# Kernel optimization log

Hardware: AMD Instinct MI355X
Metric: run time of the kernel (lower is better)

The kernel has to match this reference:

```python
import jax, jax.numpy as jnp
import numpy as np

NUM_SITES = 64
BOND_DIM = 64
PHYS_DIM = 2
BATCH = 8192
INIT_STD = 0.125  # 1/sqrt(bond_dim)
EPS_AMP = 1e-12
EPS_LOG = 1e-30


def setup_inputs() -> dict:
    key = jax.random.key(0)
    k_cfg, k_l, k_b, k_r = jax.random.split(key, 4)
    configurations = jax.random.randint(k_cfg, (BATCH, NUM_SITES), 0, PHYS_DIM, dtype=jnp.int32)
    left = jax.random.normal(k_l, (PHYS_DIM, BOND_DIM), dtype=jnp.float32) * INIT_STD
    bulk = jax.random.normal(k_b, (NUM_SITES - 2, BOND_DIM, PHYS_DIM, BOND_DIM), dtype=jnp.float32) * INIT_STD
    right = jax.random.normal(k_r, (BOND_DIM, PHYS_DIM), dtype=jnp.float32) * INIT_STD
    return {"configurations": configurations, "left": left, "bulk": bulk, "right": right}


def _psi(configurations, left, bulk, right):
    # configurations: [B, S] int; left: [d, D]; bulk: [S-2, D, d, D]; right: [D, d]
    B = configurations.shape[0]
    env0 = left[configurations[:, 0]]  # [B, D]
    cfg_mid = configurations[:, 1:-1].T  # [S-2, B]

    def step(env, xs):
        site_t, idx = xs  # site_t: [D, d, D], idx: [B]
        D = site_t.shape[0]
        # env @ site (contract left bond), then gather the per-sample physical slice
        tmp = (env @ site_t.reshape(D, -1)).reshape(B, PHYS_DIM, D)  # [B, d, D]
        env = jnp.take_along_axis(tmp, idx[:, None, None], axis=1)[:, 0, :]  # [B, D]
        return env, None

    env, _ = jax.lax.scan(step, env0, (bulk, cfg_mid))
    cols = jnp.take(right, configurations[:, -1], axis=1).T  # [B, D]
    return jnp.sum(env * cols, axis=1)  # [B]


def _log_norm(left, bulk, right):
    env0 = left.T @ left  # [D, D]  (real dtype -> conj trivial)

    def step(carry, site_t):
        env, log_scale = carry
        sm = jnp.transpose(site_t, (1, 0, 2))  # [d, D, D]
        env = jnp.einsum('pdi,de,pej->ij', sm, env, sm)  # sum_p A_p^H env A_p
        scale = jnp.maximum(jnp.max(jnp.abs(env)), EPS_LOG)
        return (env / scale, log_scale + jnp.log(scale)), None

    (env, log_scale), _ = jax.lax.scan(step, (env0, jnp.zeros((), left.dtype)), bulk)
    z = jnp.sum(right * (env @ right))
    return jnp.log(jnp.maximum(z, EPS_LOG)) + log_scale


def reference(configurations, left, bulk, right):
    psi = _psi(configurations, left, bulk, right)
    abs_sq = jnp.maximum(psi * psi, EPS_AMP)
    log_z = _log_norm(left, bulk, right)
    nll = -(jnp.log(abs_sq) - log_z)
    return jnp.mean(nll)
```

## Files before the change

kernel.cpp:

```cpp
#include <hip/hip_runtime.h>
#include <math.h>

#define NBULK 62
#define NBLK  130

typedef __attribute__((ext_vector_type(8))) short bf8_t;
typedef __attribute__((ext_vector_type(4))) float f4_t;

#define MFMA(a, b, c) __builtin_amdgcn_mfma_f32_16x16x32_bf16((a), (b), (c), 0, 0, 0)
#define LGKM_BARRIER() asm volatile("s_waitcnt lgkmcnt(0)\n\ts_barrier" ::: "memory")

__device__ __forceinline__ unsigned short f2bf(float f) {
    unsigned int u = __float_as_uint(f);
    return (unsigned short)((u + 0x7FFFu + ((u >> 16) & 1u)) >> 16);
}
__device__ __forceinline__ float bf2f(unsigned short h) {
    return __uint_as_float(((unsigned int)h) << 16);
}
__device__ __forceinline__ void gload16(const void* g, void* l) {
    __builtin_amdgcn_global_load_lds(
        (const __attribute__((address_space(1))) unsigned int*)g,
        (__attribute__((address_space(3))) unsigned int*)l, 16, 0, 0);
}

#define WS_E_OFF   1024
#define WS_B_OFF   6144
#define WS_BT_OFF  45056
#define WS_MR_OFF  1060864

extern "C" __global__ __launch_bounds__(256)
void mps_precompute(const float* __restrict__ bulkG,
                    unsigned short* __restrict__ BTg,
                    unsigned short* __restrict__ MRg,
                    float* __restrict__ wsF)
{
    __shared__ unsigned short BTl[8192];
    __shared__ unsigned short MRl[8192];
    const int s = blockIdx.x, tid = threadIdx.x;
    if (s == 0 && tid == 0) {
        wsF[0] = 0.f; wsF[1] = 0.f; wsF[2] = 0.f;
        ((int*)wsF)[3] = 0;
    }
    const float4* src = (const float4*)(bulkG + (size_t)s * 8192);
    for (int c = 0; c < 8; ++c) {
        int idx = tid + c * 256;
        float4 v = src[idx];
        int f  = idx * 4;
        int kk = f >> 7;
        int p  = (f >> 6) & 1;
        int j  = f & 63;
        unsigned short b0 = f2bf(v.x), b1 = f2bf(v.y), b2 = f2bf(v.z), b3 = f2bf(v.w);
        int n = p * 64 + kk;
        int off = n * 64 + (((j >> 3) ^ (n & 7)) << 3) + (j & 7);
        MRl[off + 0] = b0; MRl[off + 1] = b1; MRl[off + 2] = b2; MRl[off + 3] = b3;
        unsigned short bb[4] = {b0, b1, b2, b3};
        #pragma unroll
        for (int t2 = 0; t2 < 4; ++t2) {
            int n2 = p * 64 + j + t2;
            BTl[n2 * 64 + (((kk >> 3) ^ (n2 & 7)) << 3) + (kk & 7)] = bb[t2];
        }
    }
    __syncthreads();
    const uint4* bt4 = (const uint4*)BTl;
    const uint4* mr4 = (const uint4*)MRl;
    uint4* btg = (uint4*)(BTg + (size_t)s * 8192);
    uint4* mrg = (uint4*)(MRg + (size_t)s * 8192);
    for (int c = 0; c < 4; ++c) {
        int idx = tid + c * 256;
        btg[idx] = bt4[idx];
        mrg[idx] = mr4[idx];
    }
}

extern "C" __global__ __launch_bounds__(256, 1)
void mps_main(const int* __restrict__ cfgG, const float* __restrict__ leftG,
              const float* __restrict__ rightG, float* __restrict__ wsF,
              const unsigned short* __restrict__ BTg,
              const unsigned short* __restrict__ MRg,
              float* __restrict__ outG)
{
    extern __shared__ char smem[];
    unsigned short* smem16 = (unsigned short*)smem;
    const int tid  = threadIdx.x;
    const int bid  = blockIdx.x;
    const int wv   = tid >> 6;
    const int lane = tid & 63;
    const int quad = lane >> 4;
    const int ln   = lane & 15;
    const int swz  = ln & 7;

    if (bid >= 2) {
        unsigned short* Tb0 = smem16;
        unsigned short* Tb1 = Tb0 + 8192;
        unsigned short* env = Tb1 + 8192;

        const int s0  = (bid - 2) * 64;
        const int sMy = wv * 16 + ln;
        const int esw = (sMy & 7) << 3;
        unsigned short* eb = env + sMy * 64;

        unsigned long long SEL = 0ull;
        {
            const int* row = cfgG + (size_t)(s0 + sMy) * 64;
            #pragma unroll
            for (int q = 0; q < 16; ++q) {
                int4 v = *(const int4*)(row + q * 4);
                SEL |= ((unsigned long long)(v.x & 1)) << (q * 4);
                SEL |= ((unsigned long long)(v.y & 1)) << (q * 4 + 1);
                SEL |= ((unsigned long long)(v.z & 1)) << (q * 4 + 2);
                SEL |= ((unsigned long long)(v.w & 1)) << (q * 4 + 3);
            }
        }
        {
            const char* g0 = (const char*)BTg;
            for (int c = 0; c < 4; ++c) {
                int chunk = wv * 4 + c;
                gload16(g0 + chunk * 1024 + (size_t)lane * 16, (char*)Tb0 + chunk * 1024);
            }
        }
        bf8_t Ef0, Ef1;
        {
            int sel0 = (int)(SEL & 1ull);
            const float* lp = leftG + sel0 * 64;
            bf8_t t0, t1;
            #pragma unroll
            for (int j = 0; j < 8; ++j) {
                t0[j] = (short)f2bf(lp[quad * 8 + j]);
                t1[j] = (short)f2bf(lp[32 + quad * 8 + j]);
            }
            Ef0 = t0; Ef1 = t1;
        }

        for (int t = 0; t < NBULK; ++t) {
            __syncthreads();
            unsigned short* Tl = (t & 1) ? Tb1 : Tb0;
            if (t + 1 < NBULK) {
                const char* gn = (const char*)(BTg + (size_t)(t + 1) * 8192);
                char* l = (char*)((t & 1) ? Tb0 : Tb1);
                for (int c = 0; c < 4; ++c) {
                    int chunk = wv * 4 + c;
                    gload16(gn + chunk * 1024 + (size_t)lane * 16, l + chunk * 1024);
                }
            }
            f4_t a0[4], a1[4];
            #pragma unroll
            for (int mt = 0; mt < 4; ++mt) {
                const unsigned short* r0 = Tl + (mt * 16 + ln) * 64;
                const unsigned short* r1 = Tl + (64 + mt * 16 + ln) * 64;
                bf8_t A00 = *(const bf8_t*)(r0 + ((quad       ^ swz) << 3));
                bf8_t A01 = *(const bf8_t*)(r0 + (((4 + quad) ^ swz) << 3));
                bf8_t A10 = *(const bf8_t*)(r1 + ((quad       ^ swz) << 3));
                bf8_t A11 = *(const bf8_t*)(r1 + (((4 + quad) ^ swz) << 3));
                f4_t x = {0.f, 0.f, 0.f, 0.f};
                x = MFMA(A00, Ef0, x);
                x = MFMA(A01, Ef1, x);
                a0[mt] = x;
                f4_t y = {0.f, 0.f, 0.f, 0.f};
                y = MFMA(A10, Ef0, y);
                y = MFMA(A11, Ef1, y);
                a1[mt] = y;
            }
            const bool bs = ((SEL >> (t + 1)) & 1ull) != 0ull;
            #pragma unroll
            for (int mt = 0; mt < 4; ++mt) {
                ushort4 pk;
                pk.x = f2bf(bs ? a1[mt][0] : a0[mt][0]);
                pk.y = f2bf(bs ? a1[mt][1] : a0[mt][1]);
                pk.z = f2bf(bs ? a1[mt][2] : a0[mt][2]);
                pk.w = f2bf(bs ? a1[mt][3] : a0[mt][3]);
                *(ushort4*)(eb + ((mt * 16 + quad * 4) ^ esw)) = pk;
            }
            Ef0 = *(const bf8_t*)(eb + ((quad * 8)      ^ esw));
            Ef1 = *(const bf8_t*)(eb + ((quad * 8 + 32) ^ esw));
        }
        {
            const int selL = (int)((SEL >> 63) & 1ull);
            float p = 0.f;
            #pragma unroll
            for (int g2 = 0; g2 < 2; ++g2) {
                int g = quad * 2 + g2;
                bf8_t e = *(const bf8_t*)(eb + ((g * 8) ^ esw));
                #pragma unroll
                for (int j = 0; j < 8; ++j)
                    p = fmaf(bf2f((unsigned short)e[j]), rightG[(g * 8 + j) * 2 + selL], p);
            }
            p += __shfl_xor(p, 16);
            p += __shfl_xor(p, 32);
            float lp = logf(fmaxf(p * p, 1e-12f));
            lp += __shfl_xor(lp, 1); lp += __shfl_xor(lp, 2);
            lp += __shfl_xor(lp, 4); lp += __shfl_xor(lp, 8);
            if (lane == 0) atomicAdd(&wsF[0], lp);
        }
    } else {
        unsigned short* Tb0 = smem16;
        unsigned short* Tb1 = Tb0 + 8192;
        unsigned short* E   = Tb1 + 8192;
        unsigned short* St  = E + 4096;
        float* wred = (float*)(St + 8192);

        const bool fwd = (bid == 0);
        const unsigned short* srcbase = fwd ? BTg : MRg;
        {
            int i = tid >> 2, jq = tid & 3;
            for (int jj = 0; jj < 16; ++jj) {
                int j = jq * 16 + jj;
                float v;
                if (fwd) v = leftG[i] * leftG[j] + leftG[64 + i] * leftG[64 + j];
                else     v = rightG[i * 2] * rightG[j * 2] + rightG[i * 2 + 1] * rightG[j * 2 + 1];
                E[i * 64 + (j ^ ((i & 7) << 3))] = f2bf(v);
            }
        }
        {
            int st = fwd ? 0 : 61;
            const char* g = (const char*)(srcbase + (size_t)st * 8192);
            for (int c = 0; c < 4; ++c) {
                int chunk = wv * 4 + c;
                gload16(g + chunk * 1024 + (size_t)lane * 16, (char*)Tb0 + chunk * 1024);
            }
        }
        float lsum = 0.f;
        const int p   = wv >> 1;
        const int ntb = (wv & 1) * 2;
        const int mta = (wv >> 1) * 2;
        const int nta = (wv & 1) * 2;

        for (int k = 0; k < 31; ++k) {
            __syncthreads();
            unsigned short* Tl = (k & 1) ? Tb1 : Tb0;
            if (k + 1 < 31) {
                int sn = fwd ? (k + 1) : (61 - (k + 1));
                const char* g = (const char*)(srcbase + (size_t)sn * 8192);
                char* l = (char*)((k & 1) ? Tb0 : Tb1);
                for (int c = 0; c < 4; ++c) {
                    int chunk = wv * 4 + c;
                    gload16(g + chunk * 1024 + (size_t)lane * 16, l + chunk * 1024);
                }
            }
            float inv = 1.f;
            if (k > 0) {
                const float* wp = wred + ((k - 1) & 1) * 4;
                float mm = fmaxf(fmaxf(wp[0], wp[1]), fmaxf(wp[2], wp[3]));
                float sc = fmaxf(mm, 1e-30f);
                inv = 1.f / sc;
                if (tid == 0) lsum += logf(sc);
            }
            {
                bf8_t Bf[2][2];
                #pragma unroll
                for (int c = 0; c < 2; ++c) {
                    const unsigned short* rb = Tl + (p * 64 + (ntb + c) * 16 + ln) * 64;
                    Bf[c][0] = *(const bf8_t*)(rb + ((quad       ^ swz) << 3));
                    Bf[c][1] = *(const bf8_t*)(rb + (((4 + quad) ^ swz) << 3));
                }
                #pragma unroll
                for (int it = 0; it < 4; ++it) {
                    const unsigned short* er = E + (it * 16 + ln) * 64;
                    bf8_t A0 = *(const bf8_t*)(er + ((quad * 8)      ^ (swz << 3)));
                    bf8_t A1 = *(const bf8_t*)(er + ((quad * 8 + 32) ^ (swz << 3)));
                    #pragma unroll
                    for (int c = 0; c < 2; ++c) {
                        f4_t x = {0.f, 0.f, 0.f, 0.f};
                        x = MFMA(A0, Bf[c][0], x);
                        x = MFMA(A1, Bf[c][1], x);
                        int n = (ntb + c) * 16 + ln;
                        ushort4 pk;
                        pk.x = f2bf(x[0]); pk.y = f2bf(x[1]); pk.z = f2bf(x[2]); pk.w = f2bf(x[3]);
                        *(ushort4*)(St + p * 4096 + n * 64 + ((it * 16 + quad * 4) ^ ((n & 7) << 3))) = pk;
                    }
                }
            }
            LGKM_BARRIER();
            {
                f4_t o[2][2];
                #pragma unroll
                for (int mi = 0; mi < 2; ++mi)
                    #pragma unroll
                    for (int ni = 0; ni < 2; ++ni) {
                        f4_t x = {0.f, 0.f, 0.f, 0.f};
                        #pragma unroll
                        for (int pp = 0; pp < 2; ++pp) {
                            const unsigned short* ar = Tl + (pp * 64 + (mta + mi) * 16 + ln) * 64;
                            bf8_t A0 = *(const bf8_t*)(ar + ((quad       ^ swz) << 3));
                            bf8_t A1 = *(const bf8_t*)(ar + (((4 + quad) ^ swz) << 3));
                            int n2 = (nta + ni) * 16 + ln;
                            const unsigned short* br = St + pp * 4096 + n2 * 64;
                            bf8_t B0 = *(const bf8_t*)(br + ((quad * 8)      ^ ((n2 & 7) << 3)));
                            bf8_t B1 = *(const bf8_t*)(br + ((quad * 8 + 32) ^ ((n2 & 7) << 3)));
                            x = MFMA(A0, B0, x);
                            x = MFMA(A1, B1, x);
                        }
                        o[mi][ni] = x;
                    }
                float mx = 0.f;
                #pragma unroll
                for (int mi = 0; mi < 2; ++mi)
                    #pragma unroll
                    for (int ni = 0; ni < 2; ++ni) {
                        float v0 = o[mi][ni][0] * inv, v1 = o[mi][ni][1] * inv;
                        float v2 = o[mi][ni][2] * inv, v3 = o[mi][ni][3] * inv;
                        mx = fmaxf(mx, fmaxf(fmaxf(fabsf(v0), fabsf(v1)), fmaxf(fabsf(v2), fabsf(v3))));
                        ushort4 pk;
                        pk.x = f2bf(v0); pk.y = f2bf(v1); pk.z = f2bf(v2); pk.w = f2bf(v3);
                        int n2 = (nta + ni) * 16 + ln;
                        *(ushort4*)(E + n2 * 64 + (((mta + mi) * 16 + quad * 4) ^ ((n2 & 7) << 3))) = pk;
                    }
                mx = fmaxf(mx, __shfl_xor(mx, 1));  mx = fmaxf(mx, __shfl_xor(mx, 2));
                mx = fmaxf(mx, __shfl_xor(mx, 4));  mx = fmaxf(mx, __shfl_xor(mx, 8));
                mx = fmaxf(mx, __shfl_xor(mx, 16)); mx = fmaxf(mx, __shfl_xor(mx, 32));
                if (lane == 0) wred[(k & 1) * 4 + wv] = mx;
            }
        }
        __syncthreads();
        float* dst = wsF + (fwd ? WS_E_OFF : WS_B_OFF);
        for (int c = 0; c < 16; ++c) {
            int idx = tid + c * 256;
            int i = idx >> 6, j = idx & 63;
            dst[idx] = bf2f(E[i * 64 + (j ^ ((i & 7) << 3))]);
        }
        if (tid == 0) wsF[fwd ? 1 : 2] = lsum;
    }

    __syncthreads();
    __threadfence();
    __syncthreads();
    int* eflag = (int*)smem;
    if (tid == 0) {
        int old = atomicAdd((int*)wsF + 3, 1);
        eflag[0] = (old == NBLK - 1) ? 1 : 0;
    }
    __syncthreads();
    if (eflag[0]) {
        __threadfence();
        const float4* Ew = (const float4*)(wsF + WS_E_OFF);
        const float4* Bw = (const float4*)(wsF + WS_B_OFF);
        float a = 0.f;
        #pragma unroll
        for (int c = 0; c < 4; ++c) {
            int idx = tid + c * 256;
            float4 e = Ew[idx], b = Bw[idx];
            a += e.x * b.x + e.y * b.y + e.z * b.z + e.w * b.w;
        }
        #pragma unroll
        for (int off = 32; off > 0; off >>= 1)
            a += __shfl_down(a, off);
        float* ered = (float*)smem + 8;
        if ((tid & 63) == 0) ered[tid >> 6] = a;
        __syncthreads();
        if (tid == 0) {
            float z = fmaxf(ered[0] + ered[1] + ered[2] + ered[3], 1e-30f);
            float log_z = logf(z) + wsF[1] + wsF[2];
            outG[0] = log_z - wsF[0] * (1.0f / 8192.0f);
        }
    }
}

extern "C" void kernel_launch(void* const* d_in, const int* in_sizes, int n_in,
                              void* d_out, int out_size, void* d_ws, size_t ws_size,
                              hipStream_t stream)
{
    const int*   cfg   = (const int*)d_in[0];
    const float* left  = (const float*)d_in[1];
    const float* bulk  = (const float*)d_in[2];
    const float* right = (const float*)d_in[3];
    float* wsF = (float*)d_ws;
    unsigned short* BTg = (unsigned short*)((char*)d_ws + WS_BT_OFF);
    unsigned short* MRg = (unsigned short*)((char*)d_ws + WS_MR_OFF);

    mps_precompute<<<dim3(62), dim3(256), 0, stream>>>(bulk, BTg, MRg, wsF);
    mps_main<<<dim3(NBLK), dim3(256), 57472, stream>>>(cfg, left, right, wsF, BTg, MRg, (float*)d_out);
}
```

Baseline: 120.5 us.

## Switch main kernel to single-wave blocks with 32 samples each, removing barriers

The main kernel now runs one 64-lane wave per block. Each sample block handles 32 configurations (two 16-row tiles) instead of 64, and the grid doubles to 258 blocks. The two log-norm chain blocks now run as a single wave, so all __syncthreads barriers go away; explicit vmcnt waits order the async LDS prefetch instead. It also packs bf16 pairs with a hardware convert intrinsic. The aim is to cut barrier and synchronisation latency on the serial 62-step chains and spread samples across more CUs. The cost is less parallelism per block and a long serial log-norm chain done by one wave.

```diff
diff --git a/kernel.cpp b/kernel.cpp
--- a/kernel.cpp
+++ b/kernel.cpp
@@ -1,14 +1,14 @@
 #include <hip/hip_runtime.h>
+#include <hip/hip_bf16.h>
 #include <math.h>
 
 #define NBULK 62
-#define NBLK  130
+#define NBLK  258
 
 typedef __attribute__((ext_vector_type(8))) short bf8_t;
 typedef __attribute__((ext_vector_type(4))) float f4_t;
 
 #define MFMA(a, b, c) __builtin_amdgcn_mfma_f32_16x16x32_bf16((a), (b), (c), 0, 0, 0)
-#define LGKM_BARRIER() asm volatile("s_waitcnt lgkmcnt(0)\n\ts_barrier" ::: "memory")
 
 __device__ __forceinline__ unsigned short f2bf(float f) {
     unsigned int u = __float_as_uint(f);
@@ -16,6 +16,12 @@
 }
 __device__ __forceinline__ float bf2f(unsigned short h) {
     return __uint_as_float(((unsigned int)h) << 16);
+}
+__device__ __forceinline__ unsigned int pk2(float lo, float hi) {
+    __hip_bfloat162 h = __float22bfloat162_rn(make_float2(lo, hi));
+    unsigned int u;
+    __builtin_memcpy(&u, &h, 4);
+    return u;
 }
 __device__ __forceinline__ void gload16(const void* g, void* l) {
     __builtin_amdgcn_global_load_lds(
@@ -72,7 +78,7 @@
     }
 }
 
-extern "C" __global__ __launch_bounds__(256, 1)
+extern "C" __global__ __launch_bounds__(64, 1)
 void mps_main(const int* __restrict__ cfgG, const float* __restrict__ leftG,
               const float* __restrict__ rightG, float* __restrict__ wsF,
               const unsigned short* __restrict__ BTg,
@@ -81,10 +87,8 @@
 {
     extern __shared__ char smem[];
     unsigned short* smem16 = (unsigned short*)smem;
-    const int tid  = threadIdx.x;
+    const int lane = threadIdx.x;
     const int bid  = blockIdx.x;
-    const int wv   = tid >> 6;
-    const int lane = tid & 63;
     const int quad = lane >> 4;
     const int ln   = lane & 15;
     const int swz  = ln & 7;
@@ -94,260 +98,249 @@
         unsigned short* Tb1 = Tb0 + 8192;
         unsigned short* env = Tb1 + 8192;
 
-        const int s0  = (bid - 2) * 64;
-        const int sMy = wv * 16 + ln;
-        const int esw = (sMy & 7) << 3;
-        unsigned short* eb = env + sMy * 64;
-
-        unsigned long long SEL = 0ull;
-        {
-            const int* row = cfgG + (size_t)(s0 + sMy) * 64;
+        const int s0 = (bid - 2) * 32;
+        unsigned long long SEL[2];
+        #pragma unroll
+        for (int bt = 0; bt < 2; ++bt) {
+            unsigned long long m = 0ull;
+            const int* row = cfgG + (size_t)(s0 + bt * 16 + ln) * 64;
             #pragma unroll
             for (int q = 0; q < 16; ++q) {
                 int4 v = *(const int4*)(row + q * 4);
-                SEL |= ((unsigned long long)(v.x & 1)) << (q * 4);
-                SEL |= ((unsigned long long)(v.y & 1)) << (q * 4 + 1);
-                SEL |= ((unsigned long long)(v.z & 1)) << (q * 4 + 2);
-                SEL |= ((unsigned long long)(v.w & 1)) << (q * 4 + 3);
-            }
-        }
-        {
-            const char* g0 = (const char*)BTg;
-            for (int c = 0; c < 4; ++c) {
-                int chunk = wv * 4 + c;
-                gload16(g0 + chunk * 1024 + (size_t)lane * 16, (char*)Tb0 + chunk * 1024);
-            }
-        }
-        bf8_t Ef0, Ef1;
-        {
-            int sel0 = (int)(SEL & 1ull);
-            const float* lp = leftG + sel0 * 64;
+                m |= ((unsigned long long)(v.x & 1)) << (q * 4);
+                m |= ((unsigned long long)(v.y & 1)) << (q * 4 + 1);
+                m |= ((unsigned long long)(v.z & 1)) << (q * 4 + 2);
+                m |= ((unsigned long long)(v.w & 1)) << (q * 4 + 3);
+            }
+            SEL[bt] = m;
+        }
+        bf8_t Ef[2][2];
+        #pragma unroll
+        for (int bt = 0; bt < 2; ++bt) {
+            const float* lp = leftG + (int)(SEL[bt] & 1ull) * 64;
             bf8_t t0, t1;
             #pragma unroll
             for (int j = 0; j < 8; ++j) {
                 t0[j] = (short)f2bf(lp[quad * 8 + j]);
                 t1[j] = (short)f2bf(lp[32 + quad * 8 + j]);
             }
-            Ef0 = t0; Ef1 = t1;
+            Ef[bt][0] = t0; Ef[bt][1] = t1;
+        }
+        {
+            const char* g0 = (const char*)BTg;
+            #pragma unroll
+            for (int c = 0; c < 16; ++c)
+                gload16(g0 + c * 1024 + (size_t)lane * 16, (char*)Tb0 + c * 1024);
         }
 
         for (int t = 0; t < NBULK; ++t) {
-            __syncthreads();
             unsigned short* Tl = (t & 1) ? Tb1 : Tb0;
             if (t + 1 < NBULK) {
                 const char* gn = (const char*)(BTg + (size_t)(t + 1) * 8192);
                 char* l = (char*)((t & 1) ? Tb0 : Tb1);
-                for (int c = 0; c < 4; ++c) {
-                    int chunk = wv * 4 + c;
-                    gload16(gn + chunk * 1024 + (size_t)lane * 16, l + chunk * 1024);
-                }
-            }
-            f4_t a0[4], a1[4];
+                #pragma unroll
+                for (int c = 0; c < 16; ++c)
+                    gload16(gn + c * 1024 + (size_t)lane * 16, l + c * 1024);
+                asm volatile("s_waitcnt vmcnt(16)" ::: "memory");
+            } else {
+                asm volatile("s_waitcnt vmcnt(0)" ::: "memory");
+            }
+            f4_t a0[2][4], a1[2][4];
             #pragma unroll
             for (int mt = 0; mt < 4; ++mt) {
                 const unsigned short* r0 = Tl + (mt * 16 + ln) * 64;
-                const unsigned short* r1 = Tl + (64 + mt * 16 + ln) * 64;
+                const unsigned short* r1 = r0 + 4096;
                 bf8_t A00 = *(const bf8_t*)(r0 + ((quad       ^ swz) << 3));
                 bf8_t A01 = *(const bf8_t*)(r0 + (((4 + quad) ^ swz) << 3));
                 bf8_t A10 = *(const bf8_t*)(r1 + ((quad       ^ swz) << 3));
                 bf8_t A11 = *(const bf8_t*)(r1 + (((4 + quad) ^ swz) << 3));
-                f4_t x = {0.f, 0.f, 0.f, 0.f};
-                x = MFMA(A00, Ef0, x);
-                x = MFMA(A01, Ef1, x);
-                a0[mt] = x;
-                f4_t y = {0.f, 0.f, 0.f, 0.f};
-                y = MFMA(A10, Ef0, y);
-                y = MFMA(A11, Ef1, y);
-                a1[mt] = y;
-            }
-            const bool bs = ((SEL >> (t + 1)) & 1ull) != 0ull;
-            #pragma unroll
-            for (int mt = 0; mt < 4; ++mt) {
-                ushort4 pk;
-                pk.x = f2bf(bs ? a1[mt][0] : a0[mt][0]);
-                pk.y = f2bf(bs ? a1[mt][1] : a0[mt][1]);
-                pk.z = f2bf(bs ? a1[mt][2] : a0[mt][2]);
-                pk.w = f2bf(bs ? a1[mt][3] : a0[mt][3]);
-                *(ushort4*)(eb + ((mt * 16 + quad * 4) ^ esw)) = pk;
-            }
-            Ef0 = *(const bf8_t*)(eb + ((quad * 8)      ^ esw));
-            Ef1 = *(const bf8_t*)(eb + ((quad * 8 + 32) ^ esw));
+                #pragma unroll
+                for (int bt = 0; bt < 2; ++bt) {
+                    f4_t x = {0.f, 0.f, 0.f, 0.f};
+                    x = MFMA(A00, Ef[bt][0], x);
+                    x = MFMA(A01, Ef[bt][1], x);
+                    a0[bt][mt] = x;
+                    f4_t y = {0.f, 0.f, 0.f, 0.f};
+                    y = MFMA(A10, Ef[bt][0], y);
+                    y = MFMA(A11, Ef[bt][1], y);
+                    a1[bt][mt] = y;
+                }
+            }
+            #pragma unroll
+            for (int bt = 0; bt < 2; ++bt) {
+                const bool bs = ((SEL[bt] >> (t + 1)) & 1ull) != 0ull;
+                unsigned short* eb = env + (bt * 16 + ln) * 64;
+                const int esw = swz << 3;
+                #pragma unroll
+                for (int mt = 0; mt < 4; ++mt) {
+                    float v0 = bs ? a1[bt][mt][0] : a0[bt][mt][0];
+                    float v1 = bs ? a1[bt][mt][1] : a0[bt][mt][1];
+                    float v2 = bs ? a1[bt][mt][2] : a0[bt][mt][2];
+                    float v3 = bs ? a1[bt][mt][3] : a0[bt][mt][3];
+                    uint2 pk; pk.x = pk2(v0, v1); pk.y = pk2(v2, v3);
+                    *(uint2*)(eb + ((mt * 16 + quad * 4) ^ esw)) = pk;
+                }
+                Ef[bt][0] = *(const bf8_t*)(eb + ((quad * 8)      ^ esw));
+                Ef[bt][1] = *(const bf8_t*)(eb + ((quad * 8 + 32) ^ esw));
+            }
         }
         {
-            const int selL = (int)((SEL >> 63) & 1ull);
-            float p = 0.f;
-            #pragma unroll
-            for (int g2 = 0; g2 < 2; ++g2) {
-                int g = quad * 2 + g2;
-                bf8_t e = *(const bf8_t*)(eb + ((g * 8) ^ esw));
-                #pragma unroll
-                for (int j = 0; j < 8; ++j)
-                    p = fmaf(bf2f((unsigned short)e[j]), rightG[(g * 8 + j) * 2 + selL], p);
-            }
-            p += __shfl_xor(p, 16);
-            p += __shfl_xor(p, 32);
-            float lp = logf(fmaxf(p * p, 1e-12f));
-            lp += __shfl_xor(lp, 1); lp += __shfl_xor(lp, 2);
-            lp += __shfl_xor(lp, 4); lp += __shfl_xor(lp, 8);
-            if (lane == 0) atomicAdd(&wsF[0], lp);
+            float lptot = 0.f;
+            #pragma unroll
+            for (int bt = 0; bt < 2; ++bt) {
+                const unsigned short* eb = env + (bt * 16 + ln) * 64;
+                const int esw = swz << 3;
+                const int selL = (int)((SEL[bt] >> 63) & 1ull);
+                float p = 0.f;
+                #pragma unroll
+                for (int g2 = 0; g2 < 2; ++g2) {
+                    int g = quad * 2 + g2;
+                    bf8_t e = *(const bf8_t*)(eb + ((g * 8) ^ esw));
+                    #pragma unroll
+                    for (int j = 0; j < 8; ++j)
+                        p = fmaf(bf2f((unsigned short)e[j]), rightG[(g * 8 + j) * 2 + selL], p);
+                }
+                p += __shfl_xor(p, 16);
+                p += __shfl_xor(p, 32);
+                lptot += logf(fmaxf(p * p, 1e-12f));
+            }
+            lptot += __shfl_xor(lptot, 1); lptot += __shfl_xor(lptot, 2);
+            lptot += __shfl_xor(lptot, 4); lptot += __shfl_xor(lptot, 8);
+            if (lane == 0) atomicAdd(&wsF[0], lptot);
         }
     } else {
         unsigned short* Tb0 = smem16;
         unsigned short* Tb1 = Tb0 + 8192;
         unsigned short* E   = Tb1 + 8192;
         unsigned short* St  = E + 4096;
-        float* wred = (float*)(St + 8192);
 
         const bool fwd = (bid == 0);
         const unsigned short* srcbase = fwd ? BTg : MRg;
+        for (int idx = lane; idx < 4096; idx += 64) {
+            int i = idx >> 6, j = idx & 63;
+            float v;
+            if (fwd) v = leftG[i] * leftG[j] + leftG[64 + i] * leftG[64 + j];
+            else     v = rightG[i * 2] * rightG[j * 2] + rightG[i * 2 + 1] * rightG[j * 2 + 1];
+            E[i * 64 + (j ^ ((i & 7) << 3))] = f2bf(v);
+        }
         {
-            int i = tid >> 2, jq = tid & 3;
-            for (int jj = 0; jj < 16; ++jj) {
-                int j = jq * 16 + jj;
-                float v;
-                if (fwd) v = leftG[i] * leftG[j] + leftG[64 + i] * leftG[64 + j];
-                else     v = rightG[i * 2] * rightG[j * 2] + rightG[i * 2 + 1] * rightG[j * 2 + 1];
-                E[i * 64 + (j ^ ((i & 7) << 3))] = f2bf(v);
-            }
-        }
-        {
-            int st = fwd ? 0 : 61;
-            const char* g = (const char*)(srcbase + (size_t)st * 8192);
-            for (int c = 0; c < 4; ++c) {
-                int chunk = wv * 4 + c;
-                gload16(g + chunk * 1024 + (size_t)lane * 16, (char*)Tb0 + chunk * 1024);
-            }
-        }
-        float lsum = 0.f;
-        const int p   = wv >> 1;
-        const int ntb = (wv & 1) * 2;
-        const int mta = (wv >> 1) * 2;
-        const int nta = (wv & 1) * 2;
+            const char* g = (const char*)(srcbase + (size_t)(fwd ? 0 : 61) * 8192);
+            #pragma unroll
+            for (int c = 0; c < 16; ++c)
+                gload16(g + c * 1024 + (size_t)lane * 16, (char*)Tb0 + c * 1024);
+        }
+        float lsum = 0.f, inv = 1.f;
 
         for (int k = 0; k < 31; ++k) {
-            __syncthreads();
             unsigned short* Tl = (k & 1) ? Tb1 : Tb0;
             if (k + 1 < 31) {
                 int sn = fwd ? (k + 1) : (61 - (k + 1));
                 const char* g = (const char*)(srcbase + (size_t)sn * 8192);
                 char* l = (char*)((k & 1) ? Tb0 : Tb1);
-                for (int c = 0; c < 4; ++c) {
-                    int chunk = wv * 4 + c;
-                    gload16(g + chunk * 1024 + (size_t)lane * 16, l + chunk * 1024);
-                }
-            }
-            float inv = 1.f;
-            if (k > 0) {
-                const float* wp = wred + ((k - 1) & 1) * 4;
-                float mm = fmaxf(fmaxf(wp[0], wp[1]), fmaxf(wp[2], wp[3]));
-                float sc = fmaxf(mm, 1e-30f);
+                #pragma unroll
+                for (int c = 0; c < 16; ++c)
+                    gload16(g + c * 1024 + (size_t)lane * 16, l + c * 1024);
+                asm volatile("s_waitcnt vmcnt(16)" ::: "memory");
+            } else {
+                asm volatile("s_waitcnt vmcnt(0)" ::: "memory");
+            }
+            bf8_t Mf[2][4][2];
+            #pragma unroll
+            for (int p = 0; p < 2; ++p)
+                #pragma unroll
+                for (int rt = 0; rt < 4; ++rt) {
+                    const unsigned short* rb = Tl + (p * 64 + rt * 16 + ln) * 64;
+                    Mf[p][rt][0] = *(const bf8_t*)(rb + ((quad       ^ swz) << 3));
+                    Mf[p][rt][1] = *(const bf8_t*)(rb + (((4 + quad) ^ swz) << 3));
+                }
+            bf8_t Ea[4][2];
+            #pragma unroll
+            for (int it = 0; it < 4; ++it) {
+                const unsigned short* er = E + (it * 16 + ln) * 64;
+                Ea[it][0] = *(const bf8_t*)(er + ((quad * 8)      ^ (swz << 3)));
+                Ea[it][1] = *(const bf8_t*)(er + ((quad * 8 + 32) ^ (swz << 3)));
+            }
+            #pragma unroll
+            for (int p = 0; p < 2; ++p)
+                #pragma unroll
+                for (int nt = 0; nt < 4; ++nt) {
+                    int n2 = nt * 16 + ln;
+                    unsigned short* sb = St + p * 4096 + n2 * 64;
+                    #pragma unroll
+                    for (int it = 0; it < 4; ++it) {
+                        f4_t x = {0.f, 0.f, 0.f, 0.f};
+                        x = MFMA(Ea[it][0], Mf[p][nt][0], x);
+                        x = MFMA(Ea[it][1], Mf[p][nt][1], x);
+                        uint2 pk; pk.x = pk2(x[0], x[1]); pk.y = pk2(x[2], x[3]);
+                        *(uint2*)(sb + ((it * 16 + quad * 4) ^ ((n2 & 7) << 3))) = pk;
+                    }
+                }
+            bf8_t Sf[2][4][2];
+            #pragma unroll
+            for (int p = 0; p < 2; ++p)
+                #pragma unroll
+                for (int ni = 0; ni < 4; ++ni) {
+                    const unsigned short* br = St + p * 4096 + (ni * 16 + ln) * 64;
+                    Sf[p][ni][0] = *(const bf8_t*)(br + ((quad * 8)      ^ (swz << 3)));
+                    Sf[p][ni][1] = *(const bf8_t*)(br + ((quad * 8 + 32) ^ (swz << 3)));
+                }
+            float mx = 0.f;
+            #pragma unroll
+            for (int mt = 0; mt < 4; ++mt)
+                #pragma unroll
+                for (int nt2 = 0; nt2 < 4; ++nt2) {
+                    f4_t x = {0.f, 0.f, 0.f, 0.f};
+                    #pragma unroll
+                    for (int p = 0; p < 2; ++p) {
+                        x = MFMA(Mf[p][mt][0], Sf[p][nt2][0], x);
+                        x = MFMA(Mf[p][mt][1], Sf[p][nt2][1], x);
+                    }
+                    float v0 = x[0] * inv, v1 = x[1] * inv, v2 = x[2] * inv, v3 = x[3] * inv;
+                    mx = fmaxf(mx, fmaxf(fmaxf(fabsf(v0), fabsf(v1)), fmaxf(fabsf(v2), fabsf(v3))));
+                    int n2 = nt2 * 16 + ln;
+                    uint2 pk; pk.x = pk2(v0, v1); pk.y = pk2(v2, v3);
+                    *(uint2*)(E + n2 * 64 + ((mt * 16 + quad * 4) ^ ((n2 & 7) << 3))) = pk;
+                }
+            mx = fmaxf(mx, __shfl_xor(mx, 1));  mx = fmaxf(mx, __shfl_xor(mx, 2));
+            mx = fmaxf(mx, __shfl_xor(mx, 4));  mx = fmaxf(mx, __shfl_xor(mx, 8));
+            mx = fmaxf(mx, __shfl_xor(mx, 16)); mx = fmaxf(mx, __shfl_xor(mx, 32));
+            if (k < 30) {
+                float sc = fmaxf(mx, 1e-30f);
                 inv = 1.f / sc;
-                if (tid == 0) lsum += logf(sc);
-            }
-            {
-                bf8_t Bf[2][2];
-                #pragma unroll
-                for (int c = 0; c < 2; ++c) {
-                    const unsigned short* rb = Tl + (p * 64 + (ntb + c) * 16 + ln) * 64;
-                    Bf[c][0] = *(const bf8_t*)(rb + ((quad       ^ swz) << 3));
-                    Bf[c][1] = *(const bf8_t*)(rb + (((4 + quad) ^ swz) << 3));
-                }
-                #pragma unroll
-                for (int it = 0; it < 4; ++it) {
-                    const unsigned short* er = E + (it * 16 + ln) * 64;
-                    bf8_t A0 = *(const bf8_t*)(er + ((quad * 8)      ^ (swz << 3)));
-                    bf8_t A1 = *(const bf8_t*)(er + ((quad * 8 + 32) ^ (swz << 3)));
-                    #pragma unroll
-                    for (int c = 0; c < 2; ++c) {
-                        f4_t x = {0.f, 0.f, 0.f, 0.f};
-                        x = MFMA(A0, Bf[c][0], x);
-                        x = MFMA(A1, Bf[c][1], x);
-                        int n = (ntb + c) * 16 + ln;
-                        ushort4 pk;
-                        pk.x = f2bf(x[0]); pk.y = f2bf(x[1]); pk.z = f2bf(x[2]); pk.w = f2bf(x[3]);
-                        *(ushort4*)(St + p * 4096 + n * 64 + ((it * 16 + quad * 4) ^ ((n & 7) << 3))) = pk;
-                    }
-                }
-            }
-            LGKM_BARRIER();
-            {
-                f4_t o[2][2];
-                #pragma unroll
-                for (int mi = 0; mi < 2; ++mi)
-                    #pragma unroll
-                    for (int ni = 0; ni < 2; ++ni) {
-                        f4_t x = {0.f, 0.f, 0.f, 0.f};
-                        #pragma unroll
-                        for (int pp = 0; pp < 2; ++pp) {
-                            const unsigned short* ar = Tl + (pp * 64 + (mta + mi) * 16 + ln) * 64;
-                            bf8_t A0 = *(const bf8_t*)(ar + ((quad       ^ swz) << 3));
-                            bf8_t A1 = *(const bf8_t*)(ar + (((4 + quad) ^ swz) << 3));
-                            int n2 = (nta + ni) * 16 + ln;
-                            const unsigned short* br = St + pp * 4096 + n2 * 64;
-                            bf8_t B0 = *(const bf8_t*)(br + ((quad * 8)      ^ ((n2 & 7) << 3)));
-                            bf8_t B1 = *(const bf8_t*)(br + ((quad * 8 + 32) ^ ((n2 & 7) << 3)));
-                            x = MFMA(A0, B0, x);
-                            x = MFMA(A1, B1, x);
-                        }
-                        o[mi][ni] = x;
-                    }
-                float mx = 0.f;
-                #pragma unroll
-                for (int mi = 0; mi < 2; ++mi)
-                    #pragma unroll
-                    for (int ni = 0; ni < 2; ++ni) {
-                        float v0 = o[mi][ni][0] * inv, v1 = o[mi][ni][1] * inv;
-                        float v2 = o[mi][ni][2] * inv, v3 = o[mi][ni][3] * inv;
-                        mx = fmaxf(mx, fmaxf(fmaxf(fabsf(v0), fabsf(v1)), fmaxf(fabsf(v2), fabsf(v3))));
-                        ushort4 pk;
-                        pk.x = f2bf(v0); pk.y = f2bf(v1); pk.z = f2bf(v2); pk.w = f2bf(v3);
-                        int n2 = (nta + ni) * 16 + ln;
-                        *(ushort4*)(E + n2 * 64 + (((mta + mi) * 16 + quad * 4) ^ ((n2 & 7) << 3))) = pk;
-                    }
-                mx = fmaxf(mx, __shfl_xor(mx, 1));  mx = fmaxf(mx, __shfl_xor(mx, 2));
-                mx = fmaxf(mx, __shfl_xor(mx, 4));  mx = fmaxf(mx, __shfl_xor(mx, 8));
-                mx = fmaxf(mx, __shfl_xor(mx, 16)); mx = fmaxf(mx, __shfl_xor(mx, 32));
-                if (lane == 0) wred[(k & 1) * 4 + wv] = mx;
-            }
-        }
-        __syncthreads();
+                lsum += logf(sc);
+            }
+        }
         float* dst = wsF + (fwd ? WS_E_OFF : WS_B_OFF);
-        for (int c = 0; c < 16; ++c) {
-            int idx = tid + c * 256;
+        for (int idx = lane; idx < 4096; idx += 64) {
             int i = idx >> 6, j = idx & 63;
             dst[idx] = bf2f(E[i * 64 + (j ^ ((i & 7) << 3))]);
         }
-        if (tid == 0) wsF[fwd ? 1 : 2] = lsum;
-    }
-
-    __syncthreads();
+        if (lane == 0) wsF[fwd ? 1 : 2] = lsum;
+    }
+
     __threadfence();
-    __syncthreads();
-    int* eflag = (int*)smem;
-    if (tid == 0) {
+    int last = 0;
+    if (lane == 0) {
         int old = atomicAdd((int*)wsF + 3, 1);
-        eflag[0] = (old == NBLK - 1) ? 1 : 0;
-    }
-    __syncthreads();
-    if (eflag[0]) {
+        last = (old == NBLK - 1) ? 1 : 0;
+    }
+    last = __shfl(last, 0);
+    if (last) {
         __threadfence();
         const float4* Ew = (const float4*)(wsF + WS_E_OFF);
         const float4* Bw = (const float4*)(wsF + WS_B_OFF);
         float a = 0.f;
         #pragma unroll
-        for (int c = 0; c < 4; ++c) {
-            int idx = tid + c * 256;
+        for (int c = 0; c < 16; ++c) {
+            int idx = lane + c * 64;
             float4 e = Ew[idx], b = Bw[idx];
             a += e.x * b.x + e.y * b.y + e.z * b.z + e.w * b.w;
         }
-        #pragma unroll
-        for (int off = 32; off > 0; off >>= 1)
-            a += __shfl_down(a, off);
-        float* ered = (float*)smem + 8;
-        if ((tid & 63) == 0) ered[tid >> 6] = a;
-        __syncthreads();
-        if (tid == 0) {
-            float z = fmaxf(ered[0] + ered[1] + ered[2] + ered[3], 1e-30f);
+        a += __shfl_xor(a, 1);  a += __shfl_xor(a, 2);
+        a += __shfl_xor(a, 4);  a += __shfl_xor(a, 8);
+        a += __shfl_xor(a, 16); a += __shfl_xor(a, 32);
+        if (lane == 0) {
+            float z = fmaxf(a, 1e-30f);
             float log_z = logf(z) + wsF[1] + wsF[2];
             outG[0] = log_z - wsF[0] * (1.0f / 8192.0f);
         }
@@ -367,5 +360,5 @@
     unsigned short* MRg = (unsigned short*)((char*)d_ws + WS_MR_OFF);
 
     mps_precompute<<<dim3(62), dim3(256), 0, stream>>>(bulk, BTg, MRg, wsF);
-    mps_main<<<dim3(NBLK), dim3(256), 57472, stream>>>(cfg, left, right, wsF, BTg, MRg, (float*)d_out);
-}
+    mps_main<<<dim3(NBLK), dim3(64), 57344, stream>>>(cfg, left, right, wsF, BTg, MRg, (float*)d_out);
+}
```

New measurement: 172.8 us. 1.43x slower.
